# Performance work log

Measured on AMD Instinct MI355X. Metric: run time of the kernel, lower is better.

Reference implementation:

```python
import jax, jax.numpy as jnp
import numpy as np

B, T, I, H = 16384, 10, 184, 128


def _lstm_dir(x, w_ih, w_hh, b_ih, b_hh, reverse):
    # x: (B, T, I); PyTorch gate order: i, f, g, o
    h0 = jnp.zeros((x.shape[0], H), x.dtype)
    c0 = jnp.zeros((x.shape[0], H), x.dtype)
    xs = jnp.swapaxes(x, 0, 1)  # (T, B, I)
    if reverse:
        xs = xs[::-1]
    # precompute input projections for all timesteps: (T, B, 4H)
    xproj = jnp.einsum('tbi,gi->tbg', xs, w_ih) + b_ih + b_hh

    def step(carry, xp):
        h, c = carry
        gates = xp + h @ w_hh.T
        i, f, g, o = jnp.split(gates, 4, axis=-1)
        i = jax.nn.sigmoid(i); f = jax.nn.sigmoid(f)
        g = jnp.tanh(g); o = jax.nn.sigmoid(o)
        c = f * c + i * g
        h = o * jnp.tanh(c)
        return (h, c), h

    _, hs = jax.lax.scan(step, (h0, c0), xproj)  # (T, B, H)
    if reverse:
        hs = hs[::-1]
    return jnp.swapaxes(hs, 0, 1)  # (B, T, H)


def _bilstm(x, wf, whf, bf, bhf, wb, whb, bb, bhb):
    fwd = _lstm_dir(x, wf, whf, bf, bhf, False)
    bwd = _lstm_dir(x, wb, whb, bb, bhb, True)
    return jnp.concatenate([fwd, bwd], axis=-1)  # (B, T, 2H)


def setup_inputs() -> dict:
    key = jax.random.key(0)
    ks = jax.random.split(key, 21)
    s = 0.05
    d = {"x": jax.random.normal(ks[0], (B, T, I), jnp.float32)}
    def p(k, shape):
        return jax.random.normal(k, shape, jnp.float32) * s
    # rnn1: input 184 -> hidden 128, bidirectional
    d["w_ih1_f"] = p(ks[1], (4 * H, I));   d["w_hh1_f"] = p(ks[2], (4 * H, H))
    d["b_ih1_f"] = p(ks[3], (4 * H,));     d["b_hh1_f"] = p(ks[4], (4 * H,))
    d["w_ih1_b"] = p(ks[5], (4 * H, I));   d["w_hh1_b"] = p(ks[6], (4 * H, H))
    d["b_ih1_b"] = p(ks[7], (4 * H,));     d["b_hh1_b"] = p(ks[8], (4 * H,))
    # rnn2: input 256 -> hidden 128, bidirectional
    d["w_ih2_f"] = p(ks[9], (4 * H, 2 * H));  d["w_hh2_f"] = p(ks[10], (4 * H, H))
    d["b_ih2_f"] = p(ks[11], (4 * H,));       d["b_hh2_f"] = p(ks[12], (4 * H,))
    d["w_ih2_b"] = p(ks[13], (4 * H, 2 * H)); d["w_hh2_b"] = p(ks[14], (4 * H, H))
    d["b_ih2_b"] = p(ks[15], (4 * H,));       d["b_hh2_b"] = p(ks[16], (4 * H,))
    # head: Linear(512,64) -> relu -> Linear(64,1)
    d["fc1_w"] = p(ks[17], (64, 512)); d["fc1_b"] = p(ks[18], (64,))
    d["fc2_w"] = p(ks[19], (1, 64));   d["fc2_b"] = p(ks[20], (1,))
    return d


def reference(x, w_ih1_f, w_hh1_f, b_ih1_f, b_hh1_f, w_ih1_b, w_hh1_b, b_ih1_b, b_hh1_b,
              w_ih2_f, w_hh2_f, b_ih2_f, b_hh2_f, w_ih2_b, w_hh2_b, b_ih2_b, b_hh2_b,
              fc1_w, fc1_b, fc2_w, fc2_b):
    ot = x.reshape(x.shape[0], x.shape[1], -1)  # (B, T, 184)
    ot = _bilstm(ot, w_ih1_f, w_hh1_f, b_ih1_f, b_hh1_f, w_ih1_b, w_hh1_b, b_ih1_b, b_hh1_b)
    ot = _bilstm(ot, w_ih2_f, w_hh2_f, b_ih2_f, b_hh2_f, w_ih2_b, w_hh2_b, b_ih2_b, b_hh2_b)
    # permute (B, C=256, T) then MaxPool1d(kernel=5, stride=5): windows over time
    Bn = ot.shape[0]
    pooled = jnp.max(ot.reshape(Bn, T // 5, 5, 2 * H), axis=2)  # (B, 2, 256)
    pooled = jnp.transpose(pooled, (0, 2, 1)).reshape(Bn, -1)   # (B, 512) channel-major like torch
    h = jax.nn.relu(pooled @ fc1_w.T + fc1_b)
    return h @ fc2_w.T + fc2_b  # (B, 1)
```

## Files before the change

kernel.cpp:

```cpp
#include <hip/hip_runtime.h>

typedef _Float16 half8_t __attribute__((ext_vector_type(8)));
typedef _Float16 half4_t __attribute__((ext_vector_type(4)));
typedef _Float16 half2_t __attribute__((ext_vector_type(2)));
typedef float floatx4 __attribute__((ext_vector_type(4)));
typedef float float4_t __attribute__((ext_vector_type(4)));
typedef unsigned int uint4_t __attribute__((ext_vector_type(4)));

__device__ __forceinline__ float sigm_f(float v) {
  return __builtin_amdgcn_rcpf(1.f + __expf(-v));
}
__device__ __forceinline__ float tanh_f(float v) {
  return 2.f * __builtin_amdgcn_rcpf(1.f + __expf(-2.f * v)) - 1.f;
}

__device__ __forceinline__ void gl_lds16(const _Float16* g, _Float16* l) {
  __builtin_amdgcn_global_load_lds(
      (const __attribute__((address_space(1))) void*)g,
      (__attribute__((address_space(3))) void*)l, 16, 0, 0);
}

__global__ void prep_kernel(
    const float* __restrict__ wih1f, const float* __restrict__ whh1f,
    const float* __restrict__ bih1f, const float* __restrict__ bhh1f,
    const float* __restrict__ wih1b, const float* __restrict__ whh1b,
    const float* __restrict__ bih1b, const float* __restrict__ bhh1b,
    const float* __restrict__ wih2f, const float* __restrict__ whh2f,
    const float* __restrict__ bih2f, const float* __restrict__ bhh2f,
    const float* __restrict__ wih2b, const float* __restrict__ whh2b,
    const float* __restrict__ bih2b, const float* __restrict__ bhh2b,
    const float* __restrict__ fc1w,
    _Float16* __restrict__ wswz1, _Float16* __restrict__ wswz2,
    _Float16* __restrict__ wfc, float* __restrict__ biasc) {
  const int N1 = 327680, N2 = 393216, NF = 32768, NB = 2048;
  int idx = blockIdx.x * 256 + threadIdx.x;
  if (idx < N1) {
    int d = idx / 163840;
    int r = idx - d * 163840;
    int j = r & 7, lane = (r >> 3) & 63, ntg = (r >> 9) & 31, kt = r >> 14;
    int k = kt * 32 + (lane >> 4) * 8 + j;
    int n = ntg * 16 + (lane & 15);
    int oc = ((n >> 4) & 3) * 128 + (n >> 6) * 16 + (n & 15);
    const float* wih = d ? wih1b : wih1f;
    const float* whh = d ? whh1b : whh1f;
    float v = (k < 184) ? wih[oc * 184 + k]
                        : ((k < 192) ? 0.f : whh[oc * 128 + (k - 192)]);
    wswz1[idx] = (_Float16)v;
  } else if (idx < N1 + N2) {
    int r0 = idx - N1;
    int d = r0 / 196608;
    int r = r0 - d * 196608;
    int j = r & 7, lane = (r >> 3) & 63, ntg = (r >> 9) & 31, kt = r >> 14;
    int k = kt * 32 + (lane >> 4) * 8 + j;
    int n = ntg * 16 + (lane & 15);
    int oc = ((n >> 4) & 3) * 128 + (n >> 6) * 16 + (n & 15);
    const float* wih = d ? wih2b : wih2f;
    const float* whh = d ? whh2b : whh2f;
    float v = (k < 256) ? wih[oc * 256 + k] : whh[oc * 128 + (k - 256)];
    wswz2[r0] = (_Float16)v;
  } else if (idx < N1 + N2 + NF) {
    int r = idx - (N1 + N2);
    int j = r & 7, lane = (r >> 3) & 63, ntg = (r >> 9) & 3, kt = r >> 11;
    int k = kt * 32 + (lane >> 4) * 8 + j;
    int n = ntg * 16 + (lane & 15);
    wfc[r] = (_Float16)fc1w[n * 512 + k];
  } else if (idx < N1 + N2 + NF + NB) {
    int r = idx - (N1 + N2 + NF);
    int n = r & 511, d = (r >> 9) & 1, l = r >> 10;
    int oc = ((n >> 4) & 3) * 128 + (n >> 6) * 16 + (n & 15);
    const float* bi = l ? (d ? bih2b : bih2f) : (d ? bih1b : bih1f);
    const float* bh = l ? (d ? bhh2b : bhh2f) : (d ? bhh1b : bhh1f);
    biasc[r] = bi[oc] + bh[oc];
  }
}

template <int LAYER>
__global__ __launch_bounds__(512, 2) void lstm_kernel(
    const void* __restrict__ xin_v, const _Float16* __restrict__ wswz,
    const float* __restrict__ biasc, _Float16* __restrict__ outp) {
  constexpr int XT = (LAYER == 1) ? 6 : 8;
  constexpr int KT = XT + 4;
  constexpr int RKT = (LAYER == 1) ? 8 : 9;
  constexpr int LKT = KT - RKT;
  constexpr int XHALF = XT * 1024;

  __shared__ __align__(16) _Float16 Xbuf[2 * XHALF];
  __shared__ __align__(16) _Float16 Hbuf[2 * 4096];
  __shared__ __align__(16) _Float16 Wlds[LKT * 16384];

  const int tid = threadIdx.x;
  const int cs = tid >> 6;
  const int lane = tid & 63;
  const int q = lane >> 4;
  const int l15 = lane & 15;
  const int lane8 = lane * 8;
  const int dir = blockIdx.y;
  const int row0 = blockIdx.x << 5;
  const int rt0 = blockIdx.x << 1;

  const _Float16* __restrict__ wd = wswz + (size_t)dir * (KT * 16384);
  const float* __restrict__ bd = biasc + (dir << 9);

  float bias_frag[4];
#pragma unroll
  for (int nt = 0; nt < 4; ++nt) bias_frag[nt] = bd[(cs << 6) + (nt << 4) + l15];

  half8_t Wreg[RKT][4];
#pragma unroll
  for (int i = 0; i < RKT; ++i) {
    const _Float16* p = wd + (((size_t)i * 32 + (cs << 2)) * 64 + lane) * 8;
#pragma unroll
    for (int nt = 0; nt < 4; ++nt) Wreg[i][nt] = *(const half8_t*)(p + nt * 512);
  }
#pragma unroll
  for (int it = 0; it < LKT * 4; ++it) {
    int u = tid + it * 512;
    gl_lds16(wd + (size_t)RKT * 16384 + u * 8, Wlds + u * 8);
  }

  float4_t xs[3];
  auto l1_load = [&](int te) {
#pragma unroll
    for (int it = 0; it < 3; ++it) {
      int u = tid + it * 512;
      if (u < 1472) {
        int r = u / 46, c = u - r * 46;
        xs[it] = __builtin_nontemporal_load(
            (const float4_t*)((const float*)xin_v + (size_t)(row0 + r) * 1840 +
                              te * 184 + (c << 2)));
      }
    }
  };
  auto l1_write = [&](int buf) {
    _Float16* xb = Xbuf + buf * XHALF;
#pragma unroll
    for (int it = 0; it < 3; ++it) {
      int u = tid + it * 512;
      if (u < 1472) {
        int r = u / 46, c = u - r * 46, k0 = c << 2;
        half4_t hv;
        hv[0] = (_Float16)xs[it][0]; hv[1] = (_Float16)xs[it][1];
        hv[2] = (_Float16)xs[it][2]; hv[3] = (_Float16)xs[it][3];
        *(half4_t*)(xb + ((k0 >> 5) * 2 + (r >> 4)) * 512 +
                    ((k0 & 31) >> 3) * 128 + (r & 15) * 8 + (k0 & 7)) = hv;
      }
    }
  };
  auto l2_stage = [&](int buf, int te) {
    const _Float16* xf = (const _Float16*)xin_v;
    _Float16* xb = Xbuf + buf * XHALF;
#pragma unroll
    for (int it = 0; it < 2; ++it) {
      int u = tid + it * 512;
      int kt = u >> 7, mt = (u >> 6) & 1, v = u & 63;
      gl_lds16(xf + ((size_t)((rt0 + mt) * 10 + te) * 8 + kt) * 512 + v * 8,
               xb + u * 8);
    }
  };

  auto bfrag = [&](int kt, half8_t* bl) {
    if (kt < RKT) {
#pragma unroll
      for (int nt = 0; nt < 4; ++nt) bl[nt] = Wreg[kt][nt];
    } else {
#pragma unroll
      for (int nt = 0; nt < 4; ++nt)
        bl[nt] = *(const half8_t*)(Wlds + (kt - RKT) * 16384 +
                                   (((cs << 2) + nt) * 64 + lane) * 8);
    }
  };
  auto xgemm = [&](const _Float16* xb, floatx4 (*ac)[4]) {
#pragma unroll
    for (int i = 0; i < XT; ++i) {
      half8_t bl[4];
      bfrag(i, bl);
#pragma unroll
      for (int mt = 0; mt < 2; ++mt) {
        half8_t a = *(const half8_t*)(xb + i * 1024 + mt * 512 + lane8);
#pragma unroll
        for (int nt = 0; nt < 4; ++nt)
          ac[mt][nt] = __builtin_amdgcn_mfma_f32_16x16x32_f16(a, bl[nt], ac[mt][nt], 0, 0, 0);
      }
    }
  };
  auto accinit = [&](floatx4 (*ac)[4]) {
#pragma unroll
    for (int mt = 0; mt < 2; ++mt)
#pragma unroll
      for (int nt = 0; nt < 4; ++nt) {
        floatx4 b4 = {bias_frag[nt], bias_frag[nt], bias_frag[nt], bias_frag[nt]};
        ac[mt][nt] = b4;
      }
  };

  {
    uint4_t z = {0u, 0u, 0u, 0u};
    *(uint4_t*)(Hbuf + tid * 8) = z;
    if (LAYER == 1 && tid < 64) {
      half8_t hz;
#pragma unroll
      for (int j = 0; j < 8; ++j) hz[j] = (_Float16)0.f;
      int buf = tid >> 5, r = tid & 31;
      *(half8_t*)(Xbuf + buf * XHALF + (10 + (r >> 4)) * 512 + 384 + (r & 15) * 8) = hz;
    }
  }

  const int te0 = dir ? 9 : 0;
  const int te1 = dir ? 8 : 1;
  if (LAYER == 1) {
    l1_load(te0); l1_write(0);
    l1_load(te1); l1_write(1);
  } else {
    l2_stage(0, te0);
    l2_stage(1, te1);
  }

  float c_state[2][4];
#pragma unroll
  for (int mt = 0; mt < 2; ++mt)
#pragma unroll
    for (int rg = 0; rg < 4; ++rg) c_state[mt][rg] = 0.f;

  float gmax[2][2][4];
  if (LAYER == 2) {
#pragma unroll
    for (int g = 0; g < 2; ++g)
#pragma unroll
      for (int mt = 0; mt < 2; ++mt)
#pragma unroll
        for (int rg = 0; rg < 4; ++rg) gmax[g][mt][rg] = -1e30f;
  }

  __syncthreads();

  floatx4 acc[2][4];
  accinit(acc);
  xgemm(Xbuf, acc);
  __syncthreads();

  for (int t = 0; t < 10; ++t) {
    const int cur = t & 1;
    const int te = dir ? (9 - t) : t;

    if (t < 8) {
      const int te2 = dir ? (7 - t) : (t + 2);
      if (LAYER == 1) l1_load(te2);
      else l2_stage(cur, te2);
    }

    if (LAYER == 1 && t > 0) {
      const int t_prev = dir ? (10 - t) : (t - 1);
      int u = tid, hk = u >> 7, mt = (u >> 6) & 1, v = u & 63;
      __builtin_nontemporal_store(
          *(const uint4_t*)(Hbuf + cur * 4096 + u * 8),
          (uint4_t*)(outp + (((size_t)(rt0 + mt) * 10 + t_prev) * 8 + (dir << 2) + hk) * 512 +
                     v * 8));
    }

    const _Float16* hb = Hbuf + cur * 4096;
#pragma unroll
    for (int i = 0; i < 4; ++i) {
      half8_t bl[4];
      bfrag(XT + i, bl);
#pragma unroll
      for (int mt = 0; mt < 2; ++mt) {
        half8_t a = *(const half8_t*)(hb + i * 1024 + mt * 512 + lane8);
#pragma unroll
        for (int nt = 0; nt < 4; ++nt)
          acc[mt][nt] = __builtin_amdgcn_mfma_f32_16x16x32_f16(a, bl[nt], acc[mt][nt], 0, 0, 0);
      }
    }

    _Float16* hw = Hbuf + (cur ^ 1) * 4096;
#pragma unroll
    for (int mt = 0; mt < 2; ++mt) {
#pragma unroll
      for (int rg = 0; rg < 4; ++rg) {
        float ig = sigm_f(acc[mt][0][rg]);
        float fg = sigm_f(acc[mt][1][rg]);
        float gg = tanh_f(acc[mt][2][rg]);
        float og = sigm_f(acc[mt][3][rg]);
        float c = fg * c_state[mt][rg] + ig * gg;
        c_state[mt][rg] = c;
        float h = og * tanh_f(c);
        if (LAYER == 2) {
          int g = (te < 5) ? 0 : 1;
          gmax[g][mt][rg] = fmaxf(gmax[g][mt][rg], h);
        }
        hw[((cs >> 1) * 2 + mt) * 512 + (((cs & 1) * 2) + (l15 >> 3)) * 128 +
           ((q << 2) + rg) * 8 + (l15 & 7)] = (_Float16)h;
      }
    }

    if (LAYER == 1 && t < 8) l1_write(cur);

    if (t < 9) {
      floatx4 accN[2][4];
      accinit(accN);
      xgemm(Xbuf + (cur ^ 1) * XHALF, accN);
#pragma unroll
      for (int mt = 0; mt < 2; ++mt)
#pragma unroll
        for (int nt = 0; nt < 4; ++nt) acc[mt][nt] = accN[mt][nt];
    }

    __syncthreads();
  }

  if (LAYER == 1) {
    const int t_last = dir ? 0 : 9;
    int u = tid, hk = u >> 7, mt = (u >> 6) & 1, v = u & 63;
    __builtin_nontemporal_store(
        *(const uint4_t*)(Hbuf + u * 8),
        (uint4_t*)(outp + (((size_t)(rt0 + mt) * 10 + t_last) * 8 + (dir << 2) + hk) * 512 +
                   v * 8));
  } else {
    _Float16* P = Xbuf;
#pragma unroll
    for (int mt = 0; mt < 2; ++mt)
#pragma unroll
      for (int rg = 0; rg < 4; ++rg)
#pragma unroll
        for (int g = 0; g < 2; ++g)
          P[(mt * 16 + (q << 2) + rg) * 256 + ((cs << 4) + l15) * 2 + g] =
              (_Float16)gmax[g][mt][rg];
    __syncthreads();
#pragma unroll
    for (int it = 0; it < 2; ++it) {
      int u = tid + it * 512;
      int r = u >> 5, v = u & 31;
      __builtin_nontemporal_store(
          *(const uint4_t*)(P + u * 8),
          (uint4_t*)(outp + (size_t)(row0 + r) * 512 + (dir << 8) + v * 8));
    }
  }
}

__global__ __launch_bounds__(256) void fc_kernel(
    const _Float16* __restrict__ pooled_g, const _Float16* __restrict__ wfc,
    const float* __restrict__ fc1b, const float* __restrict__ fc2w,
    const float* __restrict__ fc2b, float* __restrict__ out) {
  __shared__ __align__(16) _Float16 pooled[64 * 520];
  const int tid = threadIdx.x;
  const int s0 = blockIdx.x << 6;

#pragma unroll
  for (int it = 0; it < 16; ++it) {
    int u = tid + it * 256;
    int s = u >> 6, v = u & 63;
    *(uint4_t*)(pooled + s * 520 + v * 8) =
        *(const uint4_t*)(pooled_g + (size_t)(s0 + s) * 512 + v * 8);
  }
  __syncthreads();

  const int wid = tid >> 6, lane = tid & 63, q = lane >> 4, l15 = lane & 15;
  const int m0 = wid << 4;

  const floatx4 fzero = {0.f, 0.f, 0.f, 0.f};
  floatx4 acc[4];
#pragma unroll
  for (int nt = 0; nt < 4; ++nt) acc[nt] = fzero;

#pragma unroll
  for (int kt = 0; kt < 16; ++kt) {
    half8_t a = *(const half8_t*)(pooled + (m0 + l15) * 520 + (kt << 5) + (q << 3));
#pragma unroll
    for (int nt = 0; nt < 4; ++nt) {
      half8_t b = *(const half8_t*)(wfc + ((((size_t)kt << 2) + nt) * 64 + lane) * 8);
      acc[nt] = __builtin_amdgcn_mfma_f32_16x16x32_f16(a, b, acc[nt], 0, 0, 0);
    }
  }

  float b1[4], w2[4];
#pragma unroll
  for (int nt = 0; nt < 4; ++nt) {
    b1[nt] = fc1b[(nt << 4) + l15];
    w2[nt] = fc2w[(nt << 4) + l15];
  }
  const float c2b = fc2b[0];

#pragma unroll
  for (int rg = 0; rg < 4; ++rg) {
    float v = 0.f;
#pragma unroll
    for (int nt = 0; nt < 4; ++nt)
      v += fmaxf(acc[nt][rg] + b1[nt], 0.f) * w2[nt];
    v += __shfl_xor(v, 1, 64);
    v += __shfl_xor(v, 2, 64);
    v += __shfl_xor(v, 4, 64);
    v += __shfl_xor(v, 8, 64);
    if (l15 == 0) out[s0 + m0 + (q << 2) + rg] = v + c2b;
  }
}

extern "C" void kernel_launch(void* const* d_in, const int* in_sizes, int n_in,
                              void* d_out, int out_size, void* d_ws, size_t ws_size,
                              hipStream_t stream) {
  const float* x     = (const float*)d_in[0];
  const float* wih1f = (const float*)d_in[1];
  const float* whh1f = (const float*)d_in[2];
  const float* bih1f = (const float*)d_in[3];
  const float* bhh1f = (const float*)d_in[4];
  const float* wih1b = (const float*)d_in[5];
  const float* whh1b = (const float*)d_in[6];
  const float* bih1b = (const float*)d_in[7];
  const float* bhh1b = (const float*)d_in[8];
  const float* wih2f = (const float*)d_in[9];
  const float* whh2f = (const float*)d_in[10];
  const float* bih2f = (const float*)d_in[11];
  const float* bhh2f = (const float*)d_in[12];
  const float* wih2b = (const float*)d_in[13];
  const float* whh2b = (const float*)d_in[14];
  const float* bih2b = (const float*)d_in[15];
  const float* bhh2b = (const float*)d_in[16];
  const float* fc1w  = (const float*)d_in[17];
  const float* fc1b  = (const float*)d_in[18];
  const float* fc2w  = (const float*)d_in[19];
  const float* fc2b  = (const float*)d_in[20];
  float* out = (float*)d_out;

  if (ws_size < (size_t)169287680) return;
  _Float16* pooled_g = (_Float16*)d_ws;
  _Float16* h1out = pooled_g + (size_t)8388608;
  _Float16* wswz1 = h1out + (size_t)41943040;
  _Float16* wswz2 = wswz1 + 327680;
  _Float16* wfc   = wswz2 + 393216;
  float* biasc    = (float*)(wfc + 32768);

  prep_kernel<<<2952, 256, 0, stream>>>(
      wih1f, whh1f, bih1f, bhh1f, wih1b, whh1b, bih1b, bhh1b,
      wih2f, whh2f, bih2f, bhh2f, wih2b, whh2b, bih2b, bhh2b, fc1w,
      wswz1, wswz2, wfc, biasc);
  lstm_kernel<1><<<dim3(512, 2), 512, 0, stream>>>(x, wswz1, biasc, h1out);
  lstm_kernel<2><<<dim3(512, 2), 512, 0, stream>>>(h1out, wswz2, biasc + 1024, pooled_g);
  fc_kernel<<<256, 256, 0, stream>>>(pooled_g, wfc, fc1b, fc2w, fc2b, out);
}
```

Baseline: 508.6 us.

## Double LSTM block row tile to 64 and restructure weight/activation staging

Each block now processes 64 batch rows instead of 32, halving the grid and reusing every loaded weight fragment across four M-tiles. The recurrent weights and the first four input-weight k-tiles stay in registers, and the rest come from LDS. Hbuf is single-buffered with an extra barrier. Layer 2 reads its inputs straight from global memory instead of staging them in LDS, and keeps the running max in half precision. The aim is to amortise weight loads and sync over more rows, at the cost of register pressure, fewer blocks in flight, and uncached global reads inside the inner GEMM.

Result: slower. 842.5 us (+65.7%).

```diff
diff --git a/kernel.cpp b/kernel.cpp
--- a/kernel.cpp
+++ b/kernel.cpp
@@ -80,13 +80,12 @@
     const float* __restrict__ biasc, _Float16* __restrict__ outp) {
   constexpr int XT = (LAYER == 1) ? 6 : 8;
   constexpr int KT = XT + 4;
-  constexpr int RKT = (LAYER == 1) ? 8 : 9;
-  constexpr int LKT = KT - RKT;
-  constexpr int XHALF = XT * 1024;
-
-  __shared__ __align__(16) _Float16 Xbuf[2 * XHALF];
-  __shared__ __align__(16) _Float16 Hbuf[2 * 4096];
+  constexpr int LKT = KT - 8;
+  constexpr int XBH = (LAYER == 1) ? 12288 : 8;
+
+  __shared__ __align__(16) _Float16 Hbuf[8192];
   __shared__ __align__(16) _Float16 Wlds[LKT * 16384];
+  __shared__ __align__(16) _Float16 Xbuf[2 * XBH];
 
   const int tid = threadIdx.x;
   const int cs = tid >> 6;
@@ -95,8 +94,8 @@
   const int l15 = lane & 15;
   const int lane8 = lane * 8;
   const int dir = blockIdx.y;
-  const int row0 = blockIdx.x << 5;
-  const int rt0 = blockIdx.x << 1;
+  const int row0 = blockIdx.x << 6;
+  const int rt0 = blockIdx.x << 2;
 
   const _Float16* __restrict__ wd = wswz + (size_t)dir * (KT * 16384);
   const float* __restrict__ bd = biasc + (dir << 9);
@@ -105,25 +104,72 @@
 #pragma unroll
   for (int nt = 0; nt < 4; ++nt) bias_frag[nt] = bd[(cs << 6) + (nt << 4) + l15];
 
-  half8_t Wreg[RKT][4];
-#pragma unroll
-  for (int i = 0; i < RKT; ++i) {
-    const _Float16* p = wd + (((size_t)i * 32 + (cs << 2)) * 64 + lane) * 8;
-#pragma unroll
-    for (int nt = 0; nt < 4; ++nt) Wreg[i][nt] = *(const half8_t*)(p + nt * 512);
+  half8_t Wreg[8][4];
+#pragma unroll
+  for (int s = 0; s < 8; ++s) {
+    const int ks = (s < 4) ? (XT + s) : (s - 4);
+    const _Float16* p = wd + (((size_t)ks * 32 + (cs << 2)) * 64 + lane) * 8;
+#pragma unroll
+    for (int nt = 0; nt < 4; ++nt) Wreg[s][nt] = *(const half8_t*)(p + nt * 512);
   }
 #pragma unroll
   for (int it = 0; it < LKT * 4; ++it) {
     int u = tid + it * 512;
-    gl_lds16(wd + (size_t)RKT * 16384 + u * 8, Wlds + u * 8);
-  }
-
-  float4_t xs[3];
-  auto l1_load = [&](int te) {
+    gl_lds16(wd + (size_t)4 * 16384 + u * 8, Wlds + u * 8);
+  }
+
+  auto bfrag = [&](int kt, half8_t* bl) {
+    if (kt >= XT) {
+#pragma unroll
+      for (int nt = 0; nt < 4; ++nt) bl[nt] = Wreg[kt - XT][nt];
+    } else if (kt < 4) {
+#pragma unroll
+      for (int nt = 0; nt < 4; ++nt) bl[nt] = Wreg[4 + kt][nt];
+    } else {
+#pragma unroll
+      for (int nt = 0; nt < 4; ++nt)
+        bl[nt] = *(const half8_t*)(Wlds + (kt - 4) * 16384 +
+                                   (((cs << 2) + nt) * 64 + lane) * 8);
+    }
+  };
+
+  auto accinit = [&](floatx4 (*ac)[4]) {
+#pragma unroll
+    for (int mt = 0; mt < 4; ++mt)
+#pragma unroll
+      for (int nt = 0; nt < 4; ++nt) {
+        floatx4 b4 = {bias_frag[nt], bias_frag[nt], bias_frag[nt], bias_frag[nt]};
+        ac[mt][nt] = b4;
+      }
+  };
+
+  auto xgemm = [&](int te, int buf, floatx4 (*ac)[4]) {
+#pragma unroll
+    for (int i = 0; i < XT; ++i) {
+      half8_t bl[4];
+      bfrag(i, bl);
+#pragma unroll
+      for (int mt = 0; mt < 4; ++mt) {
+        half8_t a;
+        if (LAYER == 1) {
+          a = *(const half8_t*)(Xbuf + buf * XBH + (mt * 6 + i) * 512 + lane8);
+        } else {
+          a = *(const half8_t*)((const _Float16*)xin_v +
+                                (((size_t)(rt0 + mt) * 10 + te) * 8 + i) * 512 + lane8);
+        }
+#pragma unroll
+        for (int nt = 0; nt < 4; ++nt)
+          ac[mt][nt] = __builtin_amdgcn_mfma_f32_16x16x32_f16(a, bl[nt], ac[mt][nt], 0, 0, 0);
+      }
+    }
+  };
+
+  float4_t xsA[3], xsB[3];
+  auto l1_load = [&](int te, int half, float4_t* xs) {
 #pragma unroll
     for (int it = 0; it < 3; ++it) {
-      int u = tid + it * 512;
-      if (u < 1472) {
+      int u = half * 1536 + it * 512 + tid;
+      if (u < 2944) {
         int r = u / 46, c = u - r * 46;
         xs[it] = __builtin_nontemporal_load(
             (const float4_t*)((const float*)xin_v + (size_t)(row0 + r) * 1840 +
@@ -131,149 +177,104 @@
       }
     }
   };
-  auto l1_write = [&](int buf) {
-    _Float16* xb = Xbuf + buf * XHALF;
+  auto l1_write = [&](int buf, int half, const float4_t* xs) {
+    _Float16* xb = Xbuf + buf * XBH;
 #pragma unroll
     for (int it = 0; it < 3; ++it) {
-      int u = tid + it * 512;
-      if (u < 1472) {
+      int u = half * 1536 + it * 512 + tid;
+      if (u < 2944) {
         int r = u / 46, c = u - r * 46, k0 = c << 2;
         half4_t hv;
         hv[0] = (_Float16)xs[it][0]; hv[1] = (_Float16)xs[it][1];
         hv[2] = (_Float16)xs[it][2]; hv[3] = (_Float16)xs[it][3];
-        *(half4_t*)(xb + ((k0 >> 5) * 2 + (r >> 4)) * 512 +
+        *(half4_t*)(xb + ((r >> 4) * 6 + (k0 >> 5)) * 512 +
                     ((k0 & 31) >> 3) * 128 + (r & 15) * 8 + (k0 & 7)) = hv;
       }
     }
   };
-  auto l2_stage = [&](int buf, int te) {
-    const _Float16* xf = (const _Float16*)xin_v;
-    _Float16* xb = Xbuf + buf * XHALF;
+
+  auto writeback = [&](int tp) {
 #pragma unroll
     for (int it = 0; it < 2; ++it) {
       int u = tid + it * 512;
-      int kt = u >> 7, mt = (u >> 6) & 1, v = u & 63;
-      gl_lds16(xf + ((size_t)((rt0 + mt) * 10 + te) * 8 + kt) * 512 + v * 8,
-               xb + u * 8);
-    }
-  };
-
-  auto bfrag = [&](int kt, half8_t* bl) {
-    if (kt < RKT) {
-#pragma unroll
-      for (int nt = 0; nt < 4; ++nt) bl[nt] = Wreg[kt][nt];
-    } else {
-#pragma unroll
-      for (int nt = 0; nt < 4; ++nt)
-        bl[nt] = *(const half8_t*)(Wlds + (kt - RKT) * 16384 +
-                                   (((cs << 2) + nt) * 64 + lane) * 8);
-    }
-  };
-  auto xgemm = [&](const _Float16* xb, floatx4 (*ac)[4]) {
-#pragma unroll
-    for (int i = 0; i < XT; ++i) {
-      half8_t bl[4];
-      bfrag(i, bl);
-#pragma unroll
-      for (int mt = 0; mt < 2; ++mt) {
-        half8_t a = *(const half8_t*)(xb + i * 1024 + mt * 512 + lane8);
-#pragma unroll
-        for (int nt = 0; nt < 4; ++nt)
-          ac[mt][nt] = __builtin_amdgcn_mfma_f32_16x16x32_f16(a, bl[nt], ac[mt][nt], 0, 0, 0);
-      }
-    }
-  };
-  auto accinit = [&](floatx4 (*ac)[4]) {
-#pragma unroll
-    for (int mt = 0; mt < 2; ++mt)
-#pragma unroll
-      for (int nt = 0; nt < 4; ++nt) {
-        floatx4 b4 = {bias_frag[nt], bias_frag[nt], bias_frag[nt], bias_frag[nt]};
-        ac[mt][nt] = b4;
-      }
+      int kt = u >> 8, mt = (u >> 6) & 3, v = u & 63;
+      __builtin_nontemporal_store(
+          *(const uint4_t*)(Hbuf + u * 8),
+          (uint4_t*)(outp + (((size_t)(rt0 + mt) * 10 + tp) * 8 + (dir << 2) + kt) * 512 +
+                     v * 8));
+    }
   };
 
   {
     uint4_t z = {0u, 0u, 0u, 0u};
-    *(uint4_t*)(Hbuf + tid * 8) = z;
-    if (LAYER == 1 && tid < 64) {
+#pragma unroll
+    for (int it = 0; it < 2; ++it) *(uint4_t*)(Hbuf + (tid + it * 512) * 8) = z;
+    if (LAYER == 1 && tid < 128) {
       half8_t hz;
 #pragma unroll
       for (int j = 0; j < 8; ++j) hz[j] = (_Float16)0.f;
-      int buf = tid >> 5, r = tid & 31;
-      *(half8_t*)(Xbuf + buf * XHALF + (10 + (r >> 4)) * 512 + 384 + (r & 15) * 8) = hz;
-    }
-  }
-
+      int buf = tid >> 6, r = tid & 63;
+      *(half8_t*)(Xbuf + buf * XBH + ((r >> 4) * 6 + 5) * 512 + 384 + (r & 15) * 8) = hz;
+    }
+  }
   const int te0 = dir ? 9 : 0;
   const int te1 = dir ? 8 : 1;
   if (LAYER == 1) {
-    l1_load(te0); l1_write(0);
-    l1_load(te1); l1_write(1);
-  } else {
-    l2_stage(0, te0);
-    l2_stage(1, te1);
-  }
-
-  float c_state[2][4];
-#pragma unroll
-  for (int mt = 0; mt < 2; ++mt)
+    l1_load(te0, 0, xsA); l1_load(te0, 1, xsB);
+    l1_write(0, 0, xsA);  l1_write(0, 1, xsB);
+    l1_load(te1, 0, xsA); l1_load(te1, 1, xsB);
+    l1_write(1, 0, xsA);  l1_write(1, 1, xsB);
+  }
+
+  float c_state[4][4];
+#pragma unroll
+  for (int mt = 0; mt < 4; ++mt)
 #pragma unroll
     for (int rg = 0; rg < 4; ++rg) c_state[mt][rg] = 0.f;
 
-  float gmax[2][2][4];
+  half2_t gmax[4][4];
   if (LAYER == 2) {
 #pragma unroll
-    for (int g = 0; g < 2; ++g)
-#pragma unroll
-      for (int mt = 0; mt < 2; ++mt)
-#pragma unroll
-        for (int rg = 0; rg < 4; ++rg) gmax[g][mt][rg] = -1e30f;
+    for (int mt = 0; mt < 4; ++mt)
+#pragma unroll
+      for (int rg = 0; rg < 4; ++rg) {
+        half2_t gz; gz[0] = (_Float16)(-65504.f); gz[1] = (_Float16)(-65504.f);
+        gmax[mt][rg] = gz;
+      }
   }
 
   __syncthreads();
 
-  floatx4 acc[2][4];
+  floatx4 acc[4][4];
   accinit(acc);
-  xgemm(Xbuf, acc);
-  __syncthreads();
-
+  xgemm(te0, 0, acc);
+
+#pragma unroll 1
   for (int t = 0; t < 10; ++t) {
     const int cur = t & 1;
     const int te = dir ? (9 - t) : t;
 
-    if (t < 8) {
-      const int te2 = dir ? (7 - t) : (t + 2);
-      if (LAYER == 1) l1_load(te2);
-      else l2_stage(cur, te2);
-    }
-
-    if (LAYER == 1 && t > 0) {
-      const int t_prev = dir ? (10 - t) : (t - 1);
-      int u = tid, hk = u >> 7, mt = (u >> 6) & 1, v = u & 63;
-      __builtin_nontemporal_store(
-          *(const uint4_t*)(Hbuf + cur * 4096 + u * 8),
-          (uint4_t*)(outp + (((size_t)(rt0 + mt) * 10 + t_prev) * 8 + (dir << 2) + hk) * 512 +
-                     v * 8));
-    }
-
-    const _Float16* hb = Hbuf + cur * 4096;
+    if (LAYER == 1 && t < 8) l1_load(dir ? (7 - t) : (t + 2), 0, xsA);
+    if (LAYER == 1 && t > 0) writeback(dir ? (10 - t) : (t - 1));
+
 #pragma unroll
     for (int i = 0; i < 4; ++i) {
       half8_t bl[4];
       bfrag(XT + i, bl);
 #pragma unroll
-      for (int mt = 0; mt < 2; ++mt) {
-        half8_t a = *(const half8_t*)(hb + i * 1024 + mt * 512 + lane8);
+      for (int mt = 0; mt < 4; ++mt) {
+        half8_t a = *(const half8_t*)(Hbuf + (i * 4 + mt) * 512 + lane8);
 #pragma unroll
         for (int nt = 0; nt < 4; ++nt)
           acc[mt][nt] = __builtin_amdgcn_mfma_f32_16x16x32_f16(a, bl[nt], acc[mt][nt], 0, 0, 0);
       }
     }
-
-    _Float16* hw = Hbuf + (cur ^ 1) * 4096;
-#pragma unroll
-    for (int mt = 0; mt < 2; ++mt) {
+    __syncthreads();
+
+    if (LAYER == 1 && t < 8) l1_load(dir ? (7 - t) : (t + 2), 1, xsB);
+
+#pragma unroll
+    for (int mt = 0; mt < 4; ++mt) {
 #pragma unroll
       for (int rg = 0; rg < 4; ++rg) {
         float ig = sigm_f(acc[mt][0][rg]);
@@ -283,54 +284,47 @@
         float c = fg * c_state[mt][rg] + ig * gg;
         c_state[mt][rg] = c;
         float h = og * tanh_f(c);
+        _Float16 hh = (_Float16)h;
         if (LAYER == 2) {
-          int g = (te < 5) ? 0 : 1;
-          gmax[g][mt][rg] = fmaxf(gmax[g][mt][rg], h);
+          bool lo = (te < 5);
+          half2_t hv;
+          hv[0] = lo ? hh : (_Float16)(-65504.f);
+          hv[1] = lo ? (_Float16)(-65504.f) : hh;
+          half2_t g = gmax[mt][rg];
+          g[0] = (g[0] > hv[0]) ? g[0] : hv[0];
+          g[1] = (g[1] > hv[1]) ? g[1] : hv[1];
+          gmax[mt][rg] = g;
         }
-        hw[((cs >> 1) * 2 + mt) * 512 + (((cs & 1) * 2) + (l15 >> 3)) * 128 +
-           ((q << 2) + rg) * 8 + (l15 & 7)] = (_Float16)h;
-      }
-    }
-
-    if (LAYER == 1 && t < 8) l1_write(cur);
+        Hbuf[((cs >> 1) * 4 + mt) * 512 + (((cs & 1) * 2) + (l15 >> 3)) * 128 +
+             ((q << 2) + rg) * 8 + (l15 & 7)] = hh;
+      }
+    }
+
+    if (LAYER == 1 && t < 8) { l1_write(cur, 0, xsA); l1_write(cur, 1, xsB); }
 
     if (t < 9) {
-      floatx4 accN[2][4];
-      accinit(accN);
-      xgemm(Xbuf + (cur ^ 1) * XHALF, accN);
-#pragma unroll
-      for (int mt = 0; mt < 2; ++mt)
-#pragma unroll
-        for (int nt = 0; nt < 4; ++nt) acc[mt][nt] = accN[mt][nt];
-    }
-
+      accinit(acc);
+      xgemm(dir ? (8 - t) : (t + 1), cur ^ 1, acc);
+    }
     __syncthreads();
   }
 
   if (LAYER == 1) {
-    const int t_last = dir ? 0 : 9;
-    int u = tid, hk = u >> 7, mt = (u >> 6) & 1, v = u & 63;
-    __builtin_nontemporal_store(
-        *(const uint4_t*)(Hbuf + u * 8),
-        (uint4_t*)(outp + (((size_t)(rt0 + mt) * 10 + t_last) * 8 + (dir << 2) + hk) * 512 +
-                   v * 8));
+    writeback(dir ? 0 : 9);
   } else {
-    _Float16* P = Xbuf;
-#pragma unroll
-    for (int mt = 0; mt < 2; ++mt)
+#pragma unroll
+    for (int mt = 0; mt < 4; ++mt)
 #pragma unroll
       for (int rg = 0; rg < 4; ++rg)
-#pragma unroll
-        for (int g = 0; g < 2; ++g)
-          P[(mt * 16 + (q << 2) + rg) * 256 + ((cs << 4) + l15) * 2 + g] =
-              (_Float16)gmax[g][mt][rg];
+        *(half2_t*)(Wlds + (((mt << 4) + (q << 2) + rg) << 8) +
+                    ((cs << 4) + l15) * 2) = gmax[mt][rg];
     __syncthreads();
 #pragma unroll
-    for (int it = 0; it < 2; ++it) {
+    for (int it = 0; it < 4; ++it) {
       int u = tid + it * 512;
       int r = u >> 5, v = u & 31;
       __builtin_nontemporal_store(
-          *(const uint4_t*)(P + u * 8),
+          *(const uint4_t*)(Wlds + r * 256 + v * 8),
           (uint4_t*)(outp + (size_t)(row0 + r) * 512 + (dir << 8) + v * 8));
     }
   }
@@ -431,7 +425,7 @@
       wih1f, whh1f, bih1f, bhh1f, wih1b, whh1b, bih1b, bhh1b,
       wih2f, whh2f, bih2f, bhh2f, wih2b, whh2b, bih2b, bhh2b, fc1w,
       wswz1, wswz2, wfc, biasc);
-  lstm_kernel<1><<<dim3(512, 2), 512, 0, stream>>>(x, wswz1, biasc, h1out);
-  lstm_kernel<2><<<dim3(512, 2), 512, 0, stream>>>(h1out, wswz2, biasc + 1024, pooled_g);
+  lstm_kernel<1><<<dim3(256, 2), 512, 0, stream>>>(x, wswz1, biasc, h1out);
+  lstm_kernel<2><<<dim3(256, 2), 512, 0, stream>>>(h1out, wswz2, biasc + 1024, pooled_g);
   fc_kernel<<<256, 256, 0, stream>>>(pooled_g, wfc, fc1b, fc2w, fc2b, out);
 }
```
